# Optimization experiments

Measured on AMD Instinct MI355X. Metric: run time of the kernel, lower is better.

Reference implementation:

```python
import jax, jax.numpy as jnp
import numpy as np
from jax import lax

T = 6  # max_message_length


def setup_inputs() -> dict:
    key = jax.random.key(0)
    ks = jax.random.split(key, 10)
    B, VIS, H, E, V = 8192, 512, 256, 64, 4096
    s = lambda k, shp, fan: jax.random.normal(k, shp, jnp.float32) * (1.0 / np.sqrt(fan))
    return {
        "vision_feat": jax.random.normal(ks[0], (B, VIS), jnp.float32),
        "Wv": s(ks[1], (VIS, H), VIS),
        "bv": jnp.zeros((H,), jnp.float32),
        "gru_kernel": s(ks[2], (E, 3 * H), E),          # input kernel [z|r|h]
        "gru_rec_kernel": s(ks[3], (H, 3 * H), H),      # recurrent kernel [z|r|h]
        "gru_bias_in": jnp.zeros((3 * H,), jnp.float32),
        "gru_bias_rec": jnp.zeros((3 * H,), jnp.float32),
        "Wo": s(ks[4], (H, V), H),
        "bo": jnp.zeros((V,), jnp.float32),
        "emb": s(ks[5], (V, E), E),
    }


def _gru_cell(x, h, k, rk, b_in, b_rec):
    # Keras GRUCell, reset_after=True
    H = h.shape[1]
    xm = x @ k + b_in          # [B, 3H]
    hm = h @ rk + b_rec        # [B, 3H]
    xz, xr, xh = xm[:, :H], xm[:, H:2 * H], xm[:, 2 * H:]
    hz, hr, hh = hm[:, :H], hm[:, H:2 * H], hm[:, 2 * H:]
    z = jax.nn.sigmoid(xz + hz)
    r = jax.nn.sigmoid(xr + hr)
    hh_t = jnp.tanh(xh + r * hh)
    return z * h + (1.0 - z) * hh_t


def reference(vision_feat, Wv, bv, gru_kernel, gru_rec_kernel, gru_bias_in,
              gru_bias_rec, Wo, bo, emb):
    B = vision_feat.shape[0]
    # NOTE: original code never feeds h_t back as GRU state; state is fixed.
    prev_hidden = vision_feat @ Wv + bv            # [B, H]
    cell0 = jnp.zeros((B, emb.shape[1]), vision_feat.dtype)

    def step(cell_input, _):
        h = _gru_cell(cell_input, prev_hidden, gru_kernel, gru_rec_kernel,
                      gru_bias_in, gru_bias_rec)
        lp = jax.nn.log_softmax(h @ Wo + bo, axis=1)      # [B, V]
        ent = -jnp.sum(lp * jnp.exp(lp), axis=1)          # [B]
        sym = jnp.argmax(lp, axis=1)                      # greedy (training=False)
        sel = jnp.take_along_axis(lp, sym[:, None], axis=1)[:, 0]
        return emb[sym], (sym, sel, ent, h)

    _, (syms, sels, ents, hs) = lax.scan(step, cell0, None, length=T)
    sequence = syms.T.astype(jnp.float32)                 # [B, T]
    logits = sels.T                                       # [B, T]
    entropy = jnp.mean(ents, axis=0)                      # [B]
    message_length = jnp.full((B,), float(T), jnp.float32)
    h_t = hs[-1]                                          # [B, H]
    return sequence, logits, entropy, message_length, h_t
```

## Files before the change

### kernel.cpp

```cpp
#include <hip/hip_runtime.h>
#include <hip/hip_fp16.h>
#include <math.h>


typedef __attribute__((ext_vector_type(8))) _Float16 half8v;
typedef __attribute__((ext_vector_type(4))) float f32x4;

__device__ __forceinline__ int lds_off(int row, int slot) {
    return (row << 6) + ((slot ^ (row & 3) ^ ((row >> 2) & 3)) << 4);
}

__device__ __forceinline__ void gld_lds16(const void* src, void* dst) {
    __builtin_amdgcn_global_load_lds(
        (const __attribute__((address_space(1))) void*)src,
        (__attribute__((address_space(3))) void*)dst, 16, 0, 0);
}

template<int C>
__device__ __forceinline__ float dppf(float x) {
    return __builtin_bit_cast(float, __builtin_amdgcn_update_dpp(
        __builtin_bit_cast(int, x), __builtin_bit_cast(int, x), C, 0xF, 0xF, false));
}
template<int C>
__device__ __forceinline__ int dppi(int x) {
    return __builtin_amdgcn_update_dpp(x, x, C, 0xF, 0xF, false);
}

__device__ __forceinline__ void f16split(float v, unsigned short& u0,
                                         unsigned short& u1) {
    __half a = __float2half(v);
    float f = __half2float(a);
    __half b = __float2half(v - f);
    u0 = __half_as_ushort(a);
    u1 = __half_as_ushort(b);
}

__global__ __launch_bounds__(256) void split_ew(
    const float* __restrict__ in, unsigned short* __restrict__ o0,
    unsigned short* __restrict__ o1, int n4)
{
    int i = blockIdx.x * 256 + threadIdx.x;
    if (i >= n4) return;
    float4 v = *(const float4*)&in[(size_t)i * 4];
    unsigned short a[4], b[4];
    f16split(v.x, a[0], b[0]); f16split(v.y, a[1], b[1]);
    f16split(v.z, a[2], b[2]); f16split(v.w, a[3], b[3]);
    *(uint2*)&o0[(size_t)i * 4] = *(uint2*)a;
    *(uint2*)&o1[(size_t)i * 4] = *(uint2*)b;
}

__global__ __launch_bounds__(256) void trans_split(
    const float* __restrict__ W, unsigned short* __restrict__ o0,
    unsigned short* __restrict__ o1, int N, int K)
{
    __shared__ float Ts[64][65];
    const int tid = threadIdx.x;
    const int n0 = blockIdx.x * 64, k0 = blockIdx.y * 64;
    const int ty = tid >> 2, tx = tid & 3;
    #pragma unroll
    for (int q = 0; q < 4; ++q) {
        float4 v = *(const float4*)&W[(size_t)(k0 + ty) * N + n0 + tx * 16 + q * 4];
        Ts[ty][tx * 16 + q * 4 + 0] = v.x; Ts[ty][tx * 16 + q * 4 + 1] = v.y;
        Ts[ty][tx * 16 + q * 4 + 2] = v.z; Ts[ty][tx * 16 + q * 4 + 3] = v.w;
    }
    __syncthreads();
    #pragma unroll
    for (int ii = 0; ii < 2; ++ii) {
        int item = tid + (ii << 8);
        int n = item >> 3, g = item & 7;
        unsigned short u0[8], u1[8];
        #pragma unroll
        for (int e = 0; e < 8; ++e)
            f16split(Ts[g * 8 + e][n], u0[e], u1[e]);
        size_t base = (size_t)(n0 + n) * K + k0 + g * 8;
        *(uint4*)&o0[base] = *(uint4*)u0;
        *(uint4*)&o1[base] = *(uint4*)u1;
    }
}

template<int KTOT, bool SPLIT>
__global__ __launch_bounds__(256) void mfma_gemm(
    const unsigned short* __restrict__ a0s, const unsigned short* __restrict__ a1s,
    const unsigned short* __restrict__ b0s, const unsigned short* __restrict__ b1s,
    const float* __restrict__ bias, float* __restrict__ C, int ldc,
    unsigned short* __restrict__ s0, unsigned short* __restrict__ s1)
{
    __shared__ char lds[16384];
    const int tid = threadIdx.x;
    const int w = tid >> 6, lane = tid & 63;
    const int c16 = lane & 15, rg = lane >> 4;
    const int m0 = blockIdx.y << 6, n0 = blockIdx.x << 6;
    const int arow0 = (w >> 1) << 5, brow0 = (w & 1) << 5;

    const unsigned short* segsrc = (w == 0) ? a0s : (w == 1) ? a1s
                                 : (w == 2) ? b0s : b1s;
    const int segrow0 = (w < 2) ? m0 : n0;

    f32x4 acc[2][2] = {};

    for (int t = 0; t < KTOT / 32; ++t) {
        const int k0 = t << 5;
        #pragma unroll
        for (int q = 0; q < 4; ++q) {
            int row = (q << 4) + (lane >> 2);
            int slot = (lane & 3) ^ (row & 3) ^ ((row >> 2) & 3);
            gld_lds16(segsrc + (size_t)(segrow0 + row) * KTOT + k0 + (slot << 3),
                      &lds[(w << 12) + (q << 10)]);
        }
        asm volatile("s_waitcnt vmcnt(0)" ::: "memory");
        __syncthreads();
        half8v afr[2][2], bfr[2][2];
        #pragma unroll
        for (int i = 0; i < 2; ++i) {
            int oa = lds_off(arow0 + (i << 4) + c16, rg);
            afr[i][0] = *(half8v*)&lds[oa];
            afr[i][1] = *(half8v*)&lds[4096 + oa];
            int ob = lds_off(brow0 + (i << 4) + c16, rg);
            bfr[i][0] = *(half8v*)&lds[8192 + ob];
            bfr[i][1] = *(half8v*)&lds[12288 + ob];
        }
        #pragma unroll
        for (int i = 0; i < 2; ++i)
            #pragma unroll
            for (int j = 0; j < 2; ++j) {
                f32x4 c = acc[i][j];
                c = __builtin_amdgcn_mfma_f32_16x16x32_f16(afr[i][0], bfr[j][0], c, 0, 0, 0);
                c = __builtin_amdgcn_mfma_f32_16x16x32_f16(afr[i][1], bfr[j][0], c, 0, 0, 0);
                c = __builtin_amdgcn_mfma_f32_16x16x32_f16(afr[i][0], bfr[j][1], c, 0, 0, 0);
                acc[i][j] = c;
            }
        __syncthreads();
    }

    #pragma unroll
    for (int j = 0; j < 2; ++j) {
        int col = n0 + brow0 + (j << 4) + c16;
        float bb = bias[col];
        #pragma unroll
        for (int i = 0; i < 2; ++i)
            #pragma unroll
            for (int reg = 0; reg < 4; ++reg) {
                int row = m0 + arow0 + (i << 4) + (rg << 2) + reg;
                float v = acc[i][j][reg] + bb;
                C[(size_t)row * ldc + col] = v;
                if (SPLIT) {
                    unsigned short u0, u1;
                    f16split(v, u0, u1);
                    s0[(size_t)row * ldc + col] = u0;
                    s1[(size_t)row * ldc + col] = u1;
                }
            }
    }
}

__global__ __launch_bounds__(256) void gru_fused(
    const float4* __restrict__ pstats, const float* __restrict__ emb,
    const float* __restrict__ gk, const float* __restrict__ b_in,
    const float* __restrict__ hm, const float* __restrict__ ph,
    unsigned short* __restrict__ h0, unsigned short* __restrict__ h1,
    float* __restrict__ ht_out, float* __restrict__ out_seq,
    float* __restrict__ out_sel, float* __restrict__ out_ent, int t)
{
    __shared__ float xsT[64][8];
    __shared__ int syms_lds[8];
    const int tid = threadIdx.x;
    const int row0 = blockIdx.x * 8;
    float az[8], ar[8], ah[8];
    const float bz = b_in[tid], br = b_in[256 + tid], bh = b_in[512 + tid];
    #pragma unroll
    for (int r = 0; r < 8; ++r) { az[r] = bz; ar[r] = br; ah[r] = bh; }

    if (t > 0) {
        const int r = tid >> 5, p = tid & 31;
        const int row = row0 + r;
        float4 pa = pstats[(size_t)p * 8192 + row];
        float4 pb = pstats[(size_t)(p + 32) * 8192 + row];
        float M = pa.x, S = pa.y + pb.y, Q = pa.z + pb.z;
        int A = __float_as_int(pa.w);
        { int a2 = __float_as_int(pb.w);
          if (pb.x > M || (pb.x == M && a2 < A)) { M = pb.x; A = a2; } }
        #pragma unroll
        for (int off = 1; off < 32; off <<= 1) {
            float m2 = __shfl_xor(M, off);
            float s2 = __shfl_xor(S, off);
            float q2 = __shfl_xor(Q, off);
            int   a2 = __shfl_xor(A, off);
            S += s2; Q += q2;
            if (m2 > M || (m2 == M && a2 < A)) { M = m2; A = a2; }
        }
        if (p == 0) {
            float lse = logf(S);
            float sel = M - lse;
            float ent = lse - Q / S;
            out_seq[(size_t)row * 6 + (t - 1)] = (float)A;
            out_sel[(size_t)row * 6 + (t - 1)] = sel;
            float ea = (t == 1) ? ent : (out_ent[row] + ent);
            out_ent[row] = ea;
            syms_lds[r] = A;
        }
        __syncthreads();
        for (int l = tid; l < 512; l += 256) {
            int r2 = l >> 6, e = l & 63;
            xsT[e][r2] = emb[(size_t)syms_lds[r2] * 64 + e];
        }
        __syncthreads();
        #pragma unroll 4
        for (int e = 0; e < 64; ++e) {
            float kz  = gk[e * 768 + tid];
            float kr_ = gk[e * 768 + 256 + tid];
            float kh  = gk[e * 768 + 512 + tid];
            float4 x0 = *(float4*)&xsT[e][0];
            float4 x1 = *(float4*)&xsT[e][4];
            float xv[8] = {x0.x, x0.y, x0.z, x0.w, x1.x, x1.y, x1.z, x1.w};
            #pragma unroll
            for (int r2 = 0; r2 < 8; ++r2) {
                az[r2] = fmaf(xv[r2], kz, az[r2]);
                ar[r2] = fmaf(xv[r2], kr_, ar[r2]);
                ah[r2] = fmaf(xv[r2], kh, ah[r2]);
            }
        }
    }
    #pragma unroll
    for (int r = 0; r < 8; ++r) {
        const int row = row0 + r;
        float hz  = hm[(size_t)row * 768 + tid];
        float hr  = hm[(size_t)row * 768 + 256 + tid];
        float hh  = hm[(size_t)row * 768 + 512 + tid];
        float phv = ph[(size_t)row * 256 + tid];
        float z  = 1.0f / (1.0f + __expf(-(az[r] + hz)));
        float rr = 1.0f / (1.0f + __expf(-(ar[r] + hr)));
        float ht = tanhf(ah[r] + rr * hh);
        float hv = z * phv + (1.0f - z) * ht;
        size_t idx = (size_t)row * 256 + tid;
        unsigned short u0, u1;
        f16split(hv, u0, u1);
        h0[idx] = u0; h1[idx] = u1;
        if (ht_out) ht_out[idx] = hv;
    }
}

__global__ __launch_bounds__(256, 3) void logits_mfma(
    const unsigned short* __restrict__ h0, const unsigned short* __restrict__ h1,
    const unsigned short* __restrict__ w0, const unsigned short* __restrict__ w1,
    const float* __restrict__ bo, float4* __restrict__ pstats)
{
    __shared__ char lds[32768];
    const int tid = threadIdx.x;
    const int w = tid >> 6, lane = tid & 63;
    const int c16 = lane & 15, rg = lane >> 4;
    const int m0 = blockIdx.y << 7, n0 = blockIdx.x << 7;
    const int arow0 = (w >> 1) << 6, brow0 = (w & 1) << 6;

    const unsigned short* segsrc = (w == 0) ? h0 : (w == 1) ? h1
                                 : (w == 2) ? w0 : w1;
    const int segrow0 = (w < 2) ? m0 : n0;

    f32x4 acc[4][4] = {};

    for (int t = 0; t < 8; ++t) {
        const int k0 = t << 5;
        #pragma unroll
        for (int q = 0; q < 8; ++q) {
            int row = (q << 4) + (lane >> 2);
            int slot = (lane & 3) ^ (row & 3) ^ ((row >> 2) & 3);
            gld_lds16(segsrc + (size_t)(segrow0 + row) * 256 + k0 + (slot << 3),
                      &lds[(w << 13) + (q << 10)]);
        }
        asm volatile("s_waitcnt vmcnt(0)" ::: "memory");
        __syncthreads();
        half8v afr[4][2];
        #pragma unroll
        for (int i = 0; i < 4; ++i) {
            int o = lds_off(arow0 + (i << 4) + c16, rg);
            afr[i][0] = *(half8v*)&lds[o];
            afr[i][1] = *(half8v*)&lds[8192 + o];
        }
        #pragma unroll
        for (int j = 0; j < 4; ++j) {
            int o = lds_off(brow0 + (j << 4) + c16, rg);
            half8v b0 = *(half8v*)&lds[16384 + o];
            half8v b1 = *(half8v*)&lds[24576 + o];
            #pragma unroll
            for (int i = 0; i < 4; ++i) {
                f32x4 c = acc[i][j];
                c = __builtin_amdgcn_mfma_f32_16x16x32_f16(afr[i][0], b0, c, 0, 0, 0);
                c = __builtin_amdgcn_mfma_f32_16x16x32_f16(afr[i][1], b0, c, 0, 0, 0);
                c = __builtin_amdgcn_mfma_f32_16x16x32_f16(afr[i][0], b1, c, 0, 0, 0);
                acc[i][j] = c;
            }
        }
        __syncthreads();
    }

    const int wn0 = n0 + brow0;
    float bov[4];
    #pragma unroll
    for (int j = 0; j < 4; ++j) bov[j] = bo[wn0 + j * 16 + c16];
    #pragma unroll
    for (int i = 0; i < 4; ++i) {
        #pragma unroll
        for (int reg = 0; reg < 4; ++reg) {
            float l0 = acc[i][0][reg] + bov[0];
            float l1 = acc[i][1][reg] + bov[1];
            float l2 = acc[i][2][reg] + bov[2];
            float l3 = acc[i][3][reg] + bov[3];
            float m = l0; int a = wn0 + c16;
            if (l1 > m) { m = l1; a = wn0 + 16 + c16; }
            if (l2 > m) { m = l2; a = wn0 + 32 + c16; }
            if (l3 > m) { m = l3; a = wn0 + 48 + c16; }
            float e0 = __expf(l0), e1 = __expf(l1), e2 = __expf(l2), e3 = __expf(l3);
            float s = (e0 + e1) + (e2 + e3);
            float q = fmaf(l0, e0, fmaf(l1, e1, fmaf(l2, e2, l3 * e3)));
            s += dppf<0x108>(s); s += dppf<0x104>(s);
            s += dppf<0x102>(s); s += dppf<0x101>(s);
            q += dppf<0x108>(q); q += dppf<0x104>(q);
            q += dppf<0x102>(q); q += dppf<0x101>(q);
            #define MMERGE(C) { float m2 = dppf<C>(m); int a2 = dppi<C>(a); \
                bool bt = (m2 > m) || (m2 == m && a2 < a); \
                m = bt ? m2 : m; a = bt ? a2 : a; }
            MMERGE(0x108) MMERGE(0x104) MMERGE(0x102) MMERGE(0x101)
            #undef MMERGE
            if (c16 == 0) {
                int grow = m0 + arow0 + (i << 4) + (rg << 2) + reg;
                pstats[(size_t)((blockIdx.x << 1) + (w & 1)) * 8192 + grow] =
                    make_float4(m, s, q, __int_as_float(a));
            }
        }
    }
}

__global__ __launch_bounds__(64) void finalize_kernel(
    const float4* __restrict__ pstats, float* __restrict__ out_seq,
    float* __restrict__ out_sel, float* __restrict__ out_ent,
    float* __restrict__ out_ml)
{
    const int row = blockIdx.x * 64 + threadIdx.x;
    float M = -INFINITY, S = 0.f, Q = 0.f; int A = 0;
    #pragma unroll 8
    for (int p = 0; p < 64; ++p) {
        float4 pp = pstats[(size_t)p * 8192 + row];
        S += pp.y; Q += pp.z;
        int a2 = __float_as_int(pp.w);
        if (pp.x > M || (pp.x == M && a2 < A)) { M = pp.x; A = a2; }
    }
    float lse = logf(S);
    float sel = M - lse;
    float ent = lse - Q / S;
    out_seq[(size_t)row * 6 + 5] = (float)A;
    out_sel[(size_t)row * 6 + 5] = sel;
    out_ent[row] = (out_ent[row] + ent) * (1.0f / 6.0f);
    out_ml[row] = 6.0f;
}

extern "C" void kernel_launch(void* const* d_in, const int* in_sizes, int n_in,
                              void* d_out, int out_size, void* d_ws, size_t ws_size,
                              hipStream_t stream) {
    const float* vis  = (const float*)d_in[0];
    const float* Wv   = (const float*)d_in[1];
    const float* bv   = (const float*)d_in[2];
    const float* gk   = (const float*)d_in[3];
    const float* grk  = (const float*)d_in[4];
    const float* bin  = (const float*)d_in[5];
    const float* brec = (const float*)d_in[6];
    const float* Wo   = (const float*)d_in[7];
    const float* bo   = (const float*)d_in[8];
    const float* emb  = (const float*)d_in[9];

    float* out = (float*)d_out;
    float* out_seq = out;
    float* out_sel = out + 49152;
    float* out_ent = out + 98304;
    float* out_ml  = out + 106496;
    float* out_ht  = out + 114688;

    char* ws = (char*)d_ws;
    float*          ph     = (float*)(ws);
    float*          hm     = (float*)(ws + 8388608);
    unsigned short* vis0   = (unsigned short*)(ws + 8388608);
    unsigned short* vis1   = (unsigned short*)(ws + 16777216);
    unsigned short* h0     = (unsigned short*)(ws + 33554432);
    unsigned short* h1     = (unsigned short*)(ws + 37748736);
    unsigned short* w0     = (unsigned short*)(ws + 41943040);
    unsigned short* w1     = (unsigned short*)(ws + 44040192);
    float4*         pstats = (float4*)(ws + 46137344);
    unsigned short* ph0    = (unsigned short*)(ws + 46137344);
    unsigned short* ph1    = (unsigned short*)(ws + 50331648);
    unsigned short* wv0    = (unsigned short*)(ws + 54558720);
    unsigned short* wv1    = (unsigned short*)(ws + 54820864);
    unsigned short* g0     = (unsigned short*)(ws + 55083008);
    unsigned short* g1     = (unsigned short*)(ws + 55476224);

    trans_split<<<dim3(64, 4), 256, 0, stream>>>(Wo, w0, w1, 4096, 256);
    trans_split<<<dim3(4, 8), 256, 0, stream>>>(Wv, wv0, wv1, 256, 512);
    trans_split<<<dim3(12, 4), 256, 0, stream>>>(grk, g0, g1, 768, 256);
    split_ew<<<4096, 256, 0, stream>>>(vis, vis0, vis1, 1048576);

    mfma_gemm<512, true><<<dim3(4, 128), 256, 0, stream>>>(
        vis0, vis1, wv0, wv1, bv, ph, 256, ph0, ph1);
    mfma_gemm<256, false><<<dim3(12, 128), 256, 0, stream>>>(
        ph0, ph1, g0, g1, brec, hm, 768, nullptr, nullptr);

    for (int t = 0; t < 6; ++t) {
        gru_fused<<<1024, 256, 0, stream>>>(pstats, emb, gk, bin, hm, ph,
                                            h0, h1,
                                            (t == 5) ? out_ht : nullptr,
                                            out_seq, out_sel, out_ent, t);
        logits_mfma<<<dim3(32, 64), 256, 0, stream>>>(h0, h1, w0, w1, bo, pstats);
    }
    finalize_kernel<<<128, 64, 0, stream>>>(pstats, out_seq, out_sel,
                                            out_ent, out_ml);
}
```

Before: 559.8 us.

## Use fragment-ordered LDS layout in MFMA GEMMs and fast tanh/log intrinsics

Global-to-LDS loads now place each 16-row by 32-k tile in the exact lane order the MFMA fragment reads use. Each lane then reads a contiguous 16-byte chunk at lane*16 and the XOR swizzle address math goes away. Separately, tanhf is replaced with an exp-based fast tanh and logf with __logf in the softmax-stat reductions. The layout change makes global reads less contiguous per row and changes the LDS bank pattern, and the fast math slightly lowers accuracy, which could flip argmax ties.

Result: slower. 633.6 us (+13.2%).

```diff
diff --git a/kernel.cpp b/kernel.cpp
--- a/kernel.cpp
+++ b/kernel.cpp
@@ -5,10 +5,6 @@
 
 typedef __attribute__((ext_vector_type(8))) _Float16 half8v;
 typedef __attribute__((ext_vector_type(4))) float f32x4;
-
-__device__ __forceinline__ int lds_off(int row, int slot) {
-    return (row << 6) + ((slot ^ (row & 3) ^ ((row >> 2) & 3)) << 4);
-}
 
 __device__ __forceinline__ void gld_lds16(const void* src, void* dst) {
     __builtin_amdgcn_global_load_lds(
@@ -33,6 +29,12 @@
     __half b = __float2half(v - f);
     u0 = __half_as_ushort(a);
     u1 = __half_as_ushort(b);
+}
+
+__device__ __forceinline__ float fast_tanh(float x) {
+    float t = __expf(-2.0f * fabsf(x));
+    float th = (1.0f - t) / (1.0f + t);
+    return copysignf(th, x);
 }
 
 __global__ __launch_bounds__(256) void split_ew(
@@ -95,6 +97,9 @@
     const unsigned short* segsrc = (w == 0) ? a0s : (w == 1) ? a1s
                                  : (w == 2) ? b0s : b1s;
     const int segrow0 = (w < 2) ? m0 : n0;
+    const int agb = (arow0 >> 4) << 10;
+    const int bgb = (brow0 >> 4) << 10;
+    const int lb = lane << 4;
 
     f32x4 acc[2][2] = {};
 
@@ -102,9 +107,7 @@
         const int k0 = t << 5;
         #pragma unroll
         for (int q = 0; q < 4; ++q) {
-            int row = (q << 4) + (lane >> 2);
-            int slot = (lane & 3) ^ (row & 3) ^ ((row >> 2) & 3);
-            gld_lds16(segsrc + (size_t)(segrow0 + row) * KTOT + k0 + (slot << 3),
+            gld_lds16(segsrc + (size_t)(segrow0 + (q << 4) + c16) * KTOT + k0 + rg * 8,
                       &lds[(w << 12) + (q << 10)]);
         }
         asm volatile("s_waitcnt vmcnt(0)" ::: "memory");
@@ -112,12 +115,10 @@
         half8v afr[2][2], bfr[2][2];
         #pragma unroll
         for (int i = 0; i < 2; ++i) {
-            int oa = lds_off(arow0 + (i << 4) + c16, rg);
-            afr[i][0] = *(half8v*)&lds[oa];
-            afr[i][1] = *(half8v*)&lds[4096 + oa];
-            int ob = lds_off(brow0 + (i << 4) + c16, rg);
-            bfr[i][0] = *(half8v*)&lds[8192 + ob];
-            bfr[i][1] = *(half8v*)&lds[12288 + ob];
+            afr[i][0] = *(half8v*)&lds[agb + (i << 10) + lb];
+            afr[i][1] = *(half8v*)&lds[4096 + agb + (i << 10) + lb];
+            bfr[i][0] = *(half8v*)&lds[8192 + bgb + (i << 10) + lb];
+            bfr[i][1] = *(half8v*)&lds[12288 + bgb + (i << 10) + lb];
         }
         #pragma unroll
         for (int i = 0; i < 2; ++i)
@@ -189,7 +190,7 @@
             if (m2 > M || (m2 == M && a2 < A)) { M = m2; A = a2; }
         }
         if (p == 0) {
-            float lse = logf(S);
+            float lse = __logf(S);
             float sel = M - lse;
             float ent = lse - Q / S;
             out_seq[(size_t)row * 6 + (t - 1)] = (float)A;
@@ -229,7 +230,7 @@
         float phv = ph[(size_t)row * 256 + tid];
         float z  = 1.0f / (1.0f + __expf(-(az[r] + hz)));
         float rr = 1.0f / (1.0f + __expf(-(ar[r] + hr)));
-        float ht = tanhf(ah[r] + rr * hh);
+        float ht = fast_tanh(ah[r] + rr * hh);
         float hv = z * phv + (1.0f - z) * ht;
         size_t idx = (size_t)row * 256 + tid;
         unsigned short u0, u1;
@@ -254,6 +255,9 @@
     const unsigned short* segsrc = (w == 0) ? h0 : (w == 1) ? h1
                                  : (w == 2) ? w0 : w1;
     const int segrow0 = (w < 2) ? m0 : n0;
+    const int agb = (arow0 >> 4) << 10;
+    const int bgb = (brow0 >> 4) << 10;
+    const int lb = lane << 4;
 
     f32x4 acc[4][4] = {};
 
@@ -261,9 +265,7 @@
         const int k0 = t << 5;
         #pragma unroll
         for (int q = 0; q < 8; ++q) {
-            int row = (q << 4) + (lane >> 2);
-            int slot = (lane & 3) ^ (row & 3) ^ ((row >> 2) & 3);
-            gld_lds16(segsrc + (size_t)(segrow0 + row) * 256 + k0 + (slot << 3),
+            gld_lds16(segsrc + (size_t)(segrow0 + (q << 4) + c16) * 256 + k0 + rg * 8,
                       &lds[(w << 13) + (q << 10)]);
         }
         asm volatile("s_waitcnt vmcnt(0)" ::: "memory");
@@ -271,15 +273,13 @@
         half8v afr[4][2];
         #pragma unroll
         for (int i = 0; i < 4; ++i) {
-            int o = lds_off(arow0 + (i << 4) + c16, rg);
-            afr[i][0] = *(half8v*)&lds[o];
-            afr[i][1] = *(half8v*)&lds[8192 + o];
+            afr[i][0] = *(half8v*)&lds[agb + (i << 10) + lb];
+            afr[i][1] = *(half8v*)&lds[8192 + agb + (i << 10) + lb];
         }
         #pragma unroll
         for (int j = 0; j < 4; ++j) {
-            int o = lds_off(brow0 + (j << 4) + c16, rg);
-            half8v b0 = *(half8v*)&lds[16384 + o];
-            half8v b1 = *(half8v*)&lds[24576 + o];
+            half8v b0 = *(half8v*)&lds[16384 + bgb + (j << 10) + lb];
+            half8v b1 = *(half8v*)&lds[24576 + bgb + (j << 10) + lb];
             #pragma unroll
             for (int i = 0; i < 4; ++i) {
                 f32x4 c = acc[i][j];
@@ -343,7 +343,7 @@
         int a2 = __float_as_int(pp.w);
         if (pp.x > M || (pp.x == M && a2 < A)) { M = pp.x; A = a2; }
     }
-    float lse = logf(S);
+    float lse = __logf(S);
     float sel = M - lse;
     float ent = lse - Q / S;
     out_seq[(size_t)row * 6 + 5] = (float)A;
```
